# Optimization experiments

Measured on AMD Instinct MI355X. Metric: run time of the kernel, lower is better.

## Reference

```python
import jax, jax.numpy as jnp
import numpy as np

K = 1023   # kernel_size == embedding_dim
H = 16     # out_channels (filters per sample)
E = 256    # num_embeddings
T = 8      # num_tokens
CC = 0.25  # commitment cost
EPS = np.float32(np.finfo(np.float32).eps)
DN = ('NCH', 'OIH', 'NCH')


def setup_inputs() -> dict:
    key = jax.random.key(0)
    ks = jax.random.split(key, 10)
    B, C, L = 8, 1, 8184
    D_ff = 2 * E
    X = jax.random.normal(ks[0], (B, C, L), jnp.float32)
    embedding = jax.random.uniform(ks[1], (E, K), jnp.float32, -1.0 / E, 1.0 / E)
    ffn_w1 = jax.random.normal(ks[2], (E, D_ff), jnp.float32) * 0.02
    ffn_b1 = jnp.zeros((D_ff,), jnp.float32)
    ffn_w2 = jax.random.normal(ks[3], (D_ff, E), jnp.float32) * 0.02
    ffn_b2 = jnp.zeros((E,), jnp.float32)
    ln_g = jnp.ones((E,), jnp.float32)
    ln_b = jnp.zeros((E,), jnp.float32)
    cls_w = jax.random.normal(ks[4], (E, 10), jnp.float32) * 0.02
    cls_b = jnp.zeros((10,), jnp.float32)
    return dict(X=X, embedding=embedding, ffn_w1=ffn_w1, ffn_b1=ffn_b1,
                ffn_w2=ffn_w2, ffn_b2=ffn_b2, ln_g=ln_g, ln_b=ln_b,
                cls_w=cls_w, cls_b=cls_b)


def _autocov(f):
    # f: [..., K]. FFT-based autocovariance of hann-windowed, max-normalized frame.
    n = f.shape[-1]
    fmax = jnp.max(jnp.abs(f), axis=-1, keepdims=True)
    fmax = jnp.where(fmax == 0, EPS, fmax)
    win = 0.5 * (1.0 - jnp.cos(2.0 * jnp.pi * jnp.arange(n, dtype=jnp.float32) / n))
    xw = f * win / fmax
    spec = jnp.abs(jnp.fft.rfft(xw, n=n) ** 2)   # |rfft(x)^2| == |rfft(x)|^2
    return jnp.fft.ifftshift(jnp.fft.irfft(spec, n=n), axes=-1)


def reference(X, embedding, ffn_w1, ffn_b1, ffn_w2, ffn_b2, ln_g, ln_b, cls_w, cls_b):
    B, C, L = X.shape
    # ---- encoder: extract frames at fixed linspace positions, autocovariance ----
    Lp = ((L + K - 1) // K) * K          # PadForConv(zero) length (no-op here)
    end = Lp - K - 1 - K
    positions = jnp.linspace(0.0, float(end), H).astype(jnp.int32)
    idx = positions[:, None] + jnp.arange(K)          # (H, K)
    frames = X[:, :, idx]                             # (B, C, H, K) gather
    Z = _autocov(jnp.transpose(frames, (0, 2, 1, 3)))  # (B, H, C, K)
    # ---- VQ: pairwise distances + argmin + codebook lookup ----
    flat = Z.reshape(-1, K)                           # (B*H*C, K)
    d = (jnp.sum(flat ** 2, axis=1, keepdims=True)
         + jnp.sum(embedding ** 2, axis=1)
         - 2.0 * flat @ embedding.T)                  # (B*H*C, E)
    codes = jnp.argmin(d, axis=1)
    enc = jax.nn.one_hot(codes, E, dtype=flat.dtype)
    quant = (enc @ embedding).reshape(Z.shape)
    sg = jax.lax.stop_gradient
    e_loss = jnp.mean((sg(quant) - Z) ** 2)
    q_loss = jnp.mean((quant - sg(Z)) ** 2)
    vq_loss = q_loss + CC * e_loss
    quant_st = Z + sg(quant - Z)                      # straight-through
    avg = jnp.mean(enc, axis=0)
    perplexity = jnp.exp(-jnp.sum(avg * jnp.log(avg + EPS)))
    # ---- decoder: every sample's filter bank convolved with the whole batch ----
    fmerged = quant_st.reshape(B * H, C, K)           # merge per-sample banks
    out = jax.lax.conv_general_dilated(X, fmerged, (1,), 'SAME',
                                       dimension_numbers=DN)  # (B, B*H, L)
    out = out.reshape(B, B, H, L)                     # (batch b, filter-sample i, k, L)
    sq = (out - X[:, None, :, :]) ** 2                # C==1 broadcast
    # sum_i mean_k mse_{b,l} == mean over (b,k,l) then sum over i
    recon_loss = jnp.sum(jnp.mean(sq, axis=(0, 2, 3)))
    # ---- project: conv with codebook as filters ----
    pfilt = jnp.broadcast_to(embedding[:, None, :], (E, C, K))
    proj = jax.lax.conv_general_dilated(X, pfilt, (1,), 'VALID',
                                        dimension_numbers=DN)  # (B, E, Lo)
    Lo = proj.shape[-1]
    pad = ((Lo + T - 1) // T) * T - Lo                # PadForConv(mean)
    m = jnp.mean(proj, axis=-1, keepdims=True)
    proj = jnp.concatenate([proj, jnp.broadcast_to(m, (B, E, pad))], axis=-1)
    # ---- classify ----
    x = proj.reshape(B, E, T, -1).transpose(0, 2, 3, 1)  # (B, T, t, E)
    x = jnp.max(x, axis=2)                               # (B, T, E)
    mu = jnp.mean(x, axis=-1, keepdims=True)
    var = jnp.var(x, axis=-1, keepdims=True)
    xn = (x - mu) / jnp.sqrt(var + 1e-5) * ln_g + ln_b
    hdd = jax.nn.relu(xn @ ffn_w1 + ffn_b1) @ ffn_w2 + ffn_b2
    feat = jnp.mean(hdd, axis=1)                         # (B, E)
    logits = feat @ cls_w + cls_b
    return (logits, vq_loss, recon_loss, perplexity)
```

## Files before the change

kernel.cpp:

```cpp
#include <hip/hip_runtime.h>

#define KK 1023
#define LL 8184
#define LO 7162
#define XPS 10240
#define EPSF 1.1920928955078125e-07f
#define NEG_INF (-3.4028234663852886e+38f)

typedef short bf16x8 __attribute__((ext_vector_type(8)));
typedef float f32x4 __attribute__((ext_vector_type(4)));

__device__ __constant__ int c_pos[16] = {0,409,818,1227,1636,2045,2454,2863,
                                         3273,3682,4091,4500,4909,5318,5727,6137};

__device__ __forceinline__ unsigned short f2bf(float f) {
    unsigned u = __float_as_uint(f);
    unsigned r = (u + 0x7FFFu + ((u >> 16) & 1u)) >> 16;
    return (unsigned short)r;
}
__device__ __forceinline__ int fenc(float f) {
    int u = __float_as_int(f);
    return u >= 0 ? u : (~u) ^ 0x80000000;
}
__device__ __forceinline__ float fdec(int k) {
    int u = k >= 0 ? k : ~(k ^ 0x80000000);
    return __int_as_float(u);
}
__device__ __forceinline__ void gl2lds16(const void* g, void* l) {
    __builtin_amdgcn_global_load_lds(
        (const __attribute__((address_space(1))) void*)g,
        (__attribute__((address_space(3))) void*)l, 16, 0, 0);
}

__global__ __launch_bounds__(256) void k_prep(const float* __restrict__ X,
                                              const float* __restrict__ emb,
                                              unsigned short* __restrict__ Xpad,
                                              unsigned short* __restrict__ Xodd,
                                              unsigned short* __restrict__ Ebf,
                                              float* __restrict__ Etf,
                                              float* __restrict__ enorm,
                                              int* __restrict__ hist,
                                              int* __restrict__ cmax) {
    __shared__ float red[256];
    const int q = blockIdx.x;
    const int tid = threadIdx.x;
    if (q < 32) {
        const int b = q >> 2, seg = q & 3;
        for (int i = seg * 2560 + tid; i < (seg + 1) * 2560; i += 256) {
            unsigned short v = 0, vo = 0;
            if (i >= 512 && i < 512 + LL) v = f2bf(X[b * LL + (i - 512)]);
            const int i1 = i + 1;
            if (i1 >= 512 && i1 < 512 + LL) vo = f2bf(X[b * LL + (i1 - 512)]);
            Xpad[b * XPS + i] = v;
            Xodd[b * XPS + i] = vo;
        }
    } else if (q < 288) {
        const int e = q - 32;
        const float* er = emb + e * KK;
        float nrm = 0.f;
        for (int k = tid; k < 1024; k += 256) {
            float v = (k < KK) ? er[k] : 0.f;
            Ebf[e * 1024 + k] = (k < KK) ? f2bf(v) : (unsigned short)0;
            Etf[(k >> 2) * 1024 + e * 4 + (k & 3)] = v;
            nrm = fmaf(v, v, nrm);
        }
        red[tid] = nrm;
        __syncthreads();
        for (int off = 128; off; off >>= 1) {
            if (tid < off) red[tid] += red[tid + off];
            __syncthreads();
        }
        if (tid == 0) enorm[e] = red[0];
    } else {
        const int i = (q - 288) * 256 + tid;
        cmax[i] = INT_MIN;
        if (q == 288) hist[tid] = 0;
    }
}

__global__ __launch_bounds__(256) void k_autocov(const float* __restrict__ X,
                                                 float* __restrict__ Z) {
    __shared__ __align__(16) float xw[2046];
    __shared__ float red[256];
    const int fi = blockIdx.x >> 1, half = blockIdx.x & 1;
    const int b = fi >> 4, h = fi & 15;
    const int tid = threadIdx.x;
    const float* xp = X + b * LL + c_pos[h];

    float lmax = 0.f;
    for (int j = tid; j < KK; j += 256) {
        float v = xp[j];
        xw[j] = v;
        lmax = fmaxf(lmax, fabsf(v));
    }
    red[tid] = lmax;
    __syncthreads();
    for (int off = 128; off; off >>= 1) {
        if (tid < off) red[tid] = fmaxf(red[tid], red[tid + off]);
        __syncthreads();
    }
    float fmx = red[0];
    if (fmx == 0.f) fmx = EPSF;
    __syncthreads();
    for (int j = tid; j < KK; j += 256) {
        float v = xw[j];
        float win = 0.5f * (1.0f - cosf(6.28318530717958647692f * (float)j / 1023.0f));
        float w = v * win / fmx;
        xw[j] = w;
        xw[j + KK] = w;
    }
    __syncthreads();

    const int m2 = half * 512 + 2 * tid;
    const int mh = m2 >> 1;
    const float2* X2 = (const float2*)xw;
    float a0 = 0.f, a1 = 0.f;
    float2 F = X2[mh];
#pragma unroll 4
    for (int jh = 0; jh < 511; ++jh) {
        float2 xj = X2[jh];
        float2 G = X2[mh + jh + 1];
        a0 = fmaf(xj.x, F.x, a0);
        a0 = fmaf(xj.y, F.y, a0);
        a1 = fmaf(xj.x, F.y, a1);
        a1 = fmaf(xj.y, G.x, a1);
        F = G;
    }
    float xt = xw[1022];
    a0 = fmaf(xt, F.x, a0);
    a1 = fmaf(xt, F.y, a1);
    float* zrow = Z + fi * KK;
    int i0 = m2 + 512; if (i0 >= KK) i0 -= KK;
    zrow[i0] = a0;
    if (m2 + 1 < KK) {
        int i1 = m2 + 513; if (i1 >= KK) i1 -= KK;
        zrow[i1] = a1;
    }
}

__global__ __launch_bounds__(256) void k_vq(const float* __restrict__ Z,
                                            const float4* __restrict__ Et4,
                                            const float* __restrict__ enorm,
                                            const float* __restrict__ emb,
                                            int* __restrict__ codes,
                                            int* __restrict__ hist,
                                            float* __restrict__ vq_part) {
    __shared__ float zl[KK];
    __shared__ __align__(16) float zm2[1024];
    __shared__ float rv[256];
    __shared__ int   ri[256];
    const int fi = blockIdx.x, tid = threadIdx.x;
    const float* zrow = Z + fi * KK;
    for (int t = tid; t < 1024; t += 256) {
        float z = (t < KK) ? zrow[t] : 0.f;
        if (t < KK) zl[t] = z;
        zm2[t] = -2.f * z;
    }
    __syncthreads();

    float d = enorm[tid];
    const float4* zp = (const float4*)zm2;
    const float4* ep = Et4 + tid;
#pragma unroll 8
    for (int t4 = 0; t4 < 256; ++t4) {
        float4 ev = ep[t4 * 256];
        float4 zv = zp[t4];
        d = fmaf(zv.x, ev.x, d);
        d = fmaf(zv.y, ev.y, d);
        d = fmaf(zv.z, ev.z, d);
        d = fmaf(zv.w, ev.w, d);
    }
    rv[tid] = d; ri[tid] = tid;
    __syncthreads();
    for (int off = 128; off; off >>= 1) {
        if (tid < off) {
            float v2 = rv[tid + off]; int i2 = ri[tid + off];
            if (v2 < rv[tid] || (v2 == rv[tid] && i2 < ri[tid])) { rv[tid] = v2; ri[tid] = i2; }
        }
        __syncthreads();
    }
    const int code = ri[0];
    if (tid == 0) { codes[fi] = code; atomicAdd(&hist[code], 1); }

    const float* qr = emb + code * KK;
    float s = 0.f;
    for (int t = tid; t < KK; t += 256) { float dd = qr[t] - zl[t]; s += dd * dd; }
    __syncthreads();
    rv[tid] = s;
    __syncthreads();
    for (int off = 128; off; off >>= 1) {
        if (tid < off) rv[tid] += rv[tid + off];
        __syncthreads();
    }
    if (tid == 0) vq_part[fi] = rv[0];
}

__global__ __launch_bounds__(512, 2) void k_gemm(const unsigned short* __restrict__ Xpad,
                                                 const unsigned short* __restrict__ Xodd,
                                                 const unsigned short* __restrict__ Ebf,
                                                 const int* __restrict__ codes,
                                                 const float* __restrict__ X,
                                                 float* __restrict__ psum_part,
                                                 float* __restrict__ recon_part,
                                                 int* __restrict__ cmax) {
    __shared__ __align__(16) unsigned short lds_b[16 * 1536];
    __shared__ __align__(16) unsigned short lds_a[2 * 4096];
    __shared__ float red_s[2][64][4];
    const int tid  = threadIdx.x;
    const int lane = tid & 63;
    const int c = lane & 15, g = lane >> 4;
    const int w = tid >> 6, we = w & 1, wg = w >> 1;

    const int bi = blockIdx.x;
    const bool isproj = bi < 512;
    int b, l0, e0;
    if (isproj) { b = bi >> 6; int r = bi & 63; e0 = (r >> 5) * 128; l0 = (r & 31) * 256; }
    else        { int q = bi - 512; b = q >> 5; e0 = 0; l0 = (q & 31) * 256; }
    const int xw0 = (isproj ? 512 : 0) + l0;

    {
        const unsigned short* base_e = Xpad + b * XPS;
        const unsigned short* base_o = Xodd + b * XPS;
#pragma unroll
        for (int kk = 0; kk < 2; ++kk) {
            const int wdw = 2 * w + kk;
            const unsigned short* src = (wdw & 1) ? (base_o + xw0 + wdw - 1)
                                                  : (base_e + xw0 + wdw);
#pragma unroll
            for (int p = 0; p < 3; ++p)
                gl2lds16(src + p * 512 + lane * 8, lds_b + wdw * 1536 + p * 512 + lane * 8);
        }
    }
    const int r_lds = tid >> 2, q4 = tid & 3;
    const int grow = isproj ? (e0 + r_lds) : codes[r_lds];
    const unsigned short* e_src = Ebf + grow * 1024 + q4 * 8;
    gl2lds16(e_src, lds_a + tid * 8);
    __syncthreads();

    f32x4 acc[4][4];
#pragma unroll
    for (int i = 0; i < 4; ++i)
#pragma unroll
        for (int j = 0; j < 4; ++j) acc[i][j] = (f32x4){0.f, 0.f, 0.f, 0.f};

    const char* lax = (const char*)lds_a;
    const char* lbx = (const char*)lds_b;
    const int boff0 = (wg * 4) * 3072 + 32 * c + 16 * g;
    const int aoff0 = we * 4096 + c * 64 + g * 16;

    for (int s = 0; s < 32; ++s) {
        const int cur = s & 1;
        if (s + 1 < 32)
            gl2lds16(e_src + (s + 1) * 32, lds_a + ((s + 1) & 1) * 4096 + tid * 8);
        const char* ab = lax + cur * 8192 + aoff0;
        bf16x8 af[4];
#pragma unroll
        for (int et = 0; et < 4; ++et) af[et] = *(const bf16x8*)(ab + et * 1024);
#pragma unroll
        for (int ntl = 0; ntl < 4; ++ntl) {
            bf16x8 bfrag = *(const bf16x8*)(lbx + boff0 + ntl * 3072 + 64 * s);
#pragma unroll
            for (int et = 0; et < 4; ++et)
                acc[et][ntl] = __builtin_amdgcn_mfma_f32_16x16x32_bf16(af[et], bfrag, acc[et][ntl], 0, 0, 0);
        }
        __syncthreads();
    }

    const int lseg  = l0 >> 8;
    const int lbase = l0 + wg * 4;
    if (isproj) {
        const int ch0 = lbase / 896;
#pragma unroll
        for (int et = 0; et < 4; ++et) {
#pragma unroll
            for (int r = 0; r < 4; ++r) {
                float ssum = 0.f, m0 = NEG_INF, m1 = NEG_INF;
#pragma unroll
                for (int ntl = 0; ntl < 4; ++ntl) {
                    float v = acc[et][ntl][r];
                    int l = lbase + ntl + 16 * c;
                    bool ok = l < LO;
                    ssum += ok ? v : 0.f;
                    int ch = l / 896;
                    if (ok && ch == ch0) m0 = fmaxf(m0, v);
                    if (ok && ch != ch0) m1 = fmaxf(m1, v);
                }
                ssum += __shfl_xor(ssum, 1); ssum += __shfl_xor(ssum, 2);
                ssum += __shfl_xor(ssum, 4); ssum += __shfl_xor(ssum, 8);
                m0 = fmaxf(m0, __shfl_xor(m0, 1)); m0 = fmaxf(m0, __shfl_xor(m0, 2));
                m0 = fmaxf(m0, __shfl_xor(m0, 4)); m0 = fmaxf(m0, __shfl_xor(m0, 8));
                m1 = fmaxf(m1, __shfl_xor(m1, 1)); m1 = fmaxf(m1, __shfl_xor(m1, 2));
                m1 = fmaxf(m1, __shfl_xor(m1, 4)); m1 = fmaxf(m1, __shfl_xor(m1, 8));
                if (c == 0) {
                    int eidx = et * 16 + g * 4 + r;
                    red_s[we][eidx][wg] = ssum;
                    int e = e0 + we * 64 + eidx;
                    int cb = (b * 256 + e) * 8;
                    if (m0 > NEG_INF && ch0 < 8)     atomicMax(&cmax[cb + ch0], fenc(m0));
                    if (m1 > NEG_INF && ch0 + 1 < 8) atomicMax(&cmax[cb + ch0 + 1], fenc(m1));
                }
            }
        }
    } else {
        float xv[4];
#pragma unroll
        for (int ntl = 0; ntl < 4; ++ntl) {
            int lr = lbase + ntl + 16 * c - 1;
            xv[ntl] = (lr >= 0 && lr < LL) ? X[b * LL + lr] : 0.f;
        }
#pragma unroll
        for (int et = 0; et < 4; ++et) {
#pragma unroll
            for (int r = 0; r < 4; ++r) {
                float ssum = 0.f;
#pragma unroll
                for (int ntl = 0; ntl < 4; ++ntl) {
                    int lr = lbase + ntl + 16 * c - 1;
                    bool ok = (lr >= 0) && (lr < LL);
                    float dd = ok ? (acc[et][ntl][r] - xv[ntl]) : 0.f;
                    ssum += dd * dd;
                }
                ssum += __shfl_xor(ssum, 1); ssum += __shfl_xor(ssum, 2);
                ssum += __shfl_xor(ssum, 4); ssum += __shfl_xor(ssum, 8);
                if (c == 0) red_s[we][et * 16 + g * 4 + r][wg] = ssum;
            }
        }
    }
    __syncthreads();
    if (tid < 128) {
        const int wwe = tid >> 6, eidx = tid & 63;
        float tot = red_s[wwe][eidx][0] + red_s[wwe][eidx][1]
                  + red_s[wwe][eidx][2] + red_s[wwe][eidx][3];
        if (isproj) {
            int e = e0 + wwe * 64 + eidx;
            psum_part[lseg * 2048 + b * 256 + e] = tot;
        } else {
            int f = wwe * 64 + eidx;
            recon_part[(b * 128 + f) * 32 + lseg] = tot;
        }
    }
}

__global__ __launch_bounds__(256) void k_ln(const float* __restrict__ psum_part,
                                            const int* __restrict__ cmax,
                                            const float* __restrict__ ln_g,
                                            const float* __restrict__ ln_b,
                                            float* __restrict__ xn) {
    __shared__ float red[256];
    __shared__ float red2[256];
    const int bt = blockIdx.x;
    const int t = bt & 7;
    const int b = bt >> 3;
    const int e = threadIdx.x;
    const float* ps = psum_part + b * 256 + e;
    float sm = 0.f;
#pragma unroll
    for (int s = 0; s < 32; ++s) sm += ps[s * 2048];
    float m = sm * (1.0f / 7162.0f);
    const int cb = (b * 256 + e) << 3;
    float v = (t < 7) ? fdec(cmax[cb + t]) : fmaxf(fdec(cmax[cb + 7]), m);
    red[e] = v; red2[e] = v * v;
    __syncthreads();
    for (int off = 128; off; off >>= 1) {
        if (e < off) { red[e] += red[e + off]; red2[e] += red2[e + off]; }
        __syncthreads();
    }
    float mu  = red[0] * (1.0f / 256.0f);
    float var = red2[0] * (1.0f / 256.0f) - mu * mu;
    float r = 1.0f / sqrtf(var + 1e-5f);
    xn[bt * 256 + e] = (v - mu) * r * ln_g[e] + ln_b[e];
}

__global__ __launch_bounds__(256) void k_ffn1(const float* __restrict__ xn,
                                              const float* __restrict__ w1,
                                              const float* __restrict__ b1,
                                              float* __restrict__ hbuf) {
    __shared__ float xr[256];
    __shared__ float rv[256];
    const int q = blockIdx.x;
    const int bt = q & 63, jc = q >> 6;
    const int tid = threadIdx.x;
    xr[tid] = xn[bt * 256 + tid];
    __syncthreads();
    const int jj = tid & 63, ks = tid >> 6;
    const int j = jc * 64 + jj;
    const float* wp = w1 + (ks * 64) * 512 + j;
    float a = 0.f;
#pragma unroll
    for (int ee = 0; ee < 64; ++ee) a = fmaf(xr[ks * 64 + ee], wp[ee * 512], a);
    rv[tid] = a;
    __syncthreads();
    if (tid < 64) {
        float s = rv[tid] + rv[tid + 64] + rv[tid + 128] + rv[tid + 192];
        hbuf[bt * 512 + jc * 64 + tid] = fmaxf(s + b1[jc * 64 + tid], 0.f);
    }
}

__global__ __launch_bounds__(256) void k_ffn2(const float* __restrict__ hbuf,
                                              const float* __restrict__ w2,
                                              const float* __restrict__ b2,
                                              float* __restrict__ hdd) {
    __shared__ float hr[512];
    __shared__ float rv[256];
    const int q = blockIdx.x;
    const int bt = q & 63, jc = q >> 6;
    const int tid = threadIdx.x;
    hr[tid] = hbuf[bt * 512 + tid];
    hr[tid + 256] = hbuf[bt * 512 + 256 + tid];
    __syncthreads();
    const int jj = tid & 63, ks = tid >> 6;
    const int e = jc * 64 + jj;
    const float* wp = w2 + (ks * 128) * 256 + e;
    float a = 0.f;
#pragma unroll
    for (int j = 0; j < 128; ++j) a = fmaf(hr[ks * 128 + j], wp[j * 256], a);
    rv[tid] = a;
    __syncthreads();
    if (tid < 64) {
        float s = rv[tid] + rv[tid + 64] + rv[tid + 128] + rv[tid + 192];
        hdd[bt * 256 + jc * 64 + tid] = s + b2[jc * 64 + tid];
    }
}

__global__ __launch_bounds__(256) void k_final(const float* __restrict__ hdd,
                                               const float* __restrict__ cls_w,
                                               const float* __restrict__ cls_b,
                                               const float* __restrict__ recon_part,
                                               const float* __restrict__ vq_part,
                                               const int* __restrict__ hist,
                                               float* __restrict__ out) {
    __shared__ float red[256];
    const int tid = threadIdx.x;
    if (blockIdx.x == 0) {
        __shared__ float feat[8][256];
#pragma unroll
        for (int b2 = 0; b2 < 8; ++b2) {
            float fb = 0.f;
#pragma unroll
            for (int t2 = 0; t2 < 8; ++t2) fb += hdd[(b2 * 8 + t2) * 256 + tid];
            feat[b2][tid] = fb * 0.125f;
        }
        __syncthreads();
        if (tid < 80) {
            const int b = tid / 10, k = tid % 10;
            float a = cls_b[k];
            for (int e = 0; e < 256; ++e) a = fmaf(feat[b][e], cls_w[e * 10 + k], a);
            out[tid] = a;
        }
    } else {
        float s = 0.f;
        for (int i = tid; i < 32768; i += 256) s += recon_part[i];
        red[tid] = s;
        __syncthreads();
        for (int off = 128; off; off >>= 1) { if (tid < off) red[tid] += red[tid + off]; __syncthreads(); }
        if (tid == 0) out[81] = red[0] / 1047552.0f;
        __syncthreads();
        red[tid] = (tid < 128) ? vq_part[tid] : 0.f;
        __syncthreads();
        for (int off = 128; off; off >>= 1) { if (tid < off) red[tid] += red[tid + off]; __syncthreads(); }
        if (tid == 0) out[80] = 1.25f * red[0] / 130944.0f;
        __syncthreads();
        float avg = (float)hist[tid] * (1.0f / 128.0f);
        red[tid] = avg * logf(avg + EPSF);
        __syncthreads();
        for (int off = 128; off; off >>= 1) { if (tid < off) red[tid] += red[tid + off]; __syncthreads(); }
        if (tid == 0) out[82] = expf(-red[0]);
    }
}

extern "C" void kernel_launch(void* const* d_in, const int* in_sizes, int n_in,
                              void* d_out, int out_size, void* d_ws, size_t ws_size,
                              hipStream_t stream) {
    const float* X     = (const float*)d_in[0];
    const float* emb   = (const float*)d_in[1];
    const float* w1    = (const float*)d_in[2];
    const float* b1    = (const float*)d_in[3];
    const float* w2    = (const float*)d_in[4];
    const float* b2    = (const float*)d_in[5];
    const float* ln_g  = (const float*)d_in[6];
    const float* ln_b  = (const float*)d_in[7];
    const float* cls_w = (const float*)d_in[8];
    const float* cls_b = (const float*)d_in[9];
    float* out = (float*)d_out;

    float* Z            = (float*)d_ws;
    float* vq_part      = Z + 130944;
    float* xnbuf        = vq_part + 128;
    float* hdd          = xnbuf + 16384;
    float* psum_part    = hdd + 16384;
    float* recon_part   = psum_part + 65536;
    int*   cmaxb        = (int*)(recon_part + 32768);
    int*   codes        = cmaxb + 16384;
    int*   hist         = codes + 128;
    unsigned short* Xpad = (unsigned short*)(hist + 256);
    unsigned short* Xodd = Xpad + 8 * XPS;
    unsigned short* Ebf  = Xodd + 8 * XPS;
    float* Etf           = (float*)(Ebf + 256 * 1024);
    float* enorm         = Etf + 256 * 1024;
    float* hbuf          = enorm + 256;

    k_prep   <<<dim3(352), dim3(256), 0, stream>>>(X, emb, Xpad, Xodd, Ebf, Etf, enorm, hist, cmaxb);
    k_autocov<<<dim3(256), dim3(256), 0, stream>>>(X, Z);
    k_vq     <<<dim3(128), dim3(256), 0, stream>>>(Z, (const float4*)Etf, enorm, emb, codes, hist, vq_part);
    k_gemm   <<<dim3(768), dim3(512), 0, stream>>>(Xpad, Xodd, Ebf, codes, X, psum_part, recon_part, cmaxb);
    k_ln     <<<dim3(64),  dim3(256), 0, stream>>>(psum_part, cmaxb, ln_g, ln_b, xnbuf);
    k_ffn1   <<<dim3(512), dim3(256), 0, stream>>>(xnbuf, w1, b1, hbuf);
    k_ffn2   <<<dim3(256), dim3(256), 0, stream>>>(hbuf, w2, b2, hdd);
    k_final  <<<dim3(2),   dim3(256), 0, stream>>>(hdd, cls_w, cls_b, recon_part, vq_part, hist, out);
}
```

Baseline: 145.4 us.

## Halve GEMM tile rows to cut LDS and registers and raise occupancy

Shrinks the k_gemm tile from 128 to 64 codebook rows per block and restructures the shifted-X LDS staging into 8 windows of 1280 elements, so each wave holds 2x4 accumulators instead of 4x4. The block count doubles to 1536 and launch bounds request 6 blocks per CU, aiming for more resident waves to hide LDS and global latency. In exchange, each B-fragment is reused across fewer rows, more X data is reloaded per row, and more atomics and partial writes are issued.

```diff
diff --git a/kernel.cpp b/kernel.cpp
--- a/kernel.cpp
+++ b/kernel.cpp
@@ -195,7 +195,7 @@
     if (tid == 0) vq_part[fi] = rv[0];
 }
 
-__global__ __launch_bounds__(512, 2) void k_gemm(const unsigned short* __restrict__ Xpad,
+__global__ __launch_bounds__(512, 6) void k_gemm(const unsigned short* __restrict__ Xpad,
                                                  const unsigned short* __restrict__ Xodd,
                                                  const unsigned short* __restrict__ Ebf,
                                                  const int* __restrict__ codes,
@@ -203,65 +203,64 @@
                                                  float* __restrict__ psum_part,
                                                  float* __restrict__ recon_part,
                                                  int* __restrict__ cmax) {
-    __shared__ __align__(16) unsigned short lds_b[16 * 1536];
-    __shared__ __align__(16) unsigned short lds_a[2 * 4096];
-    __shared__ float red_s[2][64][4];
+    __shared__ __align__(16) unsigned short lds_b[8 * 1280];
+    __shared__ __align__(16) unsigned short lds_a[2 * 2048];
+    __shared__ float red_s[64][4];
     const int tid  = threadIdx.x;
     const int lane = tid & 63;
     const int c = lane & 15, g = lane >> 4;
     const int w = tid >> 6, we = w & 1, wg = w >> 1;
 
     const int bi = blockIdx.x;
-    const bool isproj = bi < 512;
-    int b, l0, e0;
-    if (isproj) { b = bi >> 6; int r = bi & 63; e0 = (r >> 5) * 128; l0 = (r & 31) * 256; }
-    else        { int q = bi - 512; b = q >> 5; e0 = 0; l0 = (q & 31) * 256; }
+    const bool isproj = bi < 1024;
+    int b, l0, row0;
+    if (isproj) { b = bi >> 7; int r = bi & 127; row0 = (r >> 5) * 64; l0 = (r & 31) * 256; }
+    else        { int q = bi - 1024; b = q >> 6; int r = q & 63; row0 = (r >> 5) * 64; l0 = (r & 31) * 256; }
     const int xw0 = (isproj ? 512 : 0) + l0;
 
     {
-        const unsigned short* base_e = Xpad + b * XPS;
-        const unsigned short* base_o = Xodd + b * XPS;
-#pragma unroll
-        for (int kk = 0; kk < 2; ++kk) {
-            const int wdw = 2 * w + kk;
-            const unsigned short* src = (wdw & 1) ? (base_o + xw0 + wdw - 1)
-                                                  : (base_e + xw0 + wdw);
-#pragma unroll
-            for (int p = 0; p < 3; ++p)
-                gl2lds16(src + p * 512 + lane * 8, lds_b + wdw * 1536 + p * 512 + lane * 8);
-        }
-    }
-    const int r_lds = tid >> 2, q4 = tid & 3;
-    const int grow = isproj ? (e0 + r_lds) : codes[r_lds];
-    const unsigned short* e_src = Ebf + grow * 1024 + q4 * 8;
-    gl2lds16(e_src, lds_a + tid * 8);
-    __syncthreads();
-
-    f32x4 acc[4][4];
-#pragma unroll
-    for (int i = 0; i < 4; ++i)
+        const unsigned short* base_e = Xpad + b * XPS + xw0;
+        const unsigned short* base_o = Xodd + b * XPS + xw0;
+        for (int k = tid; k < 1280; k += 512) {
+            const int wdw = k / 160;
+            const int p = k - wdw * 160;
+            const unsigned short* src = (wdw & 1) ? (base_o + wdw - 1 + p * 8)
+                                                  : (base_e + wdw + p * 8);
+            gl2lds16(src, lds_b + k * 8);
+        }
+    }
+    const unsigned short* e_src = nullptr;
+    if (tid < 256) {
+        const int r_lds = tid >> 2, q4 = tid & 3;
+        const int grow = isproj ? (row0 + r_lds) : codes[row0 + r_lds];
+        e_src = Ebf + grow * 1024 + q4 * 8;
+        gl2lds16(e_src, lds_a + tid * 8);
+    }
+    __syncthreads();
+
+    f32x4 acc[2][4];
+#pragma unroll
+    for (int i = 0; i < 2; ++i)
 #pragma unroll
         for (int j = 0; j < 4; ++j) acc[i][j] = (f32x4){0.f, 0.f, 0.f, 0.f};
 
     const char* lax = (const char*)lds_a;
     const char* lbx = (const char*)lds_b;
-    const int boff0 = (wg * 4) * 3072 + 32 * c + 16 * g;
-    const int aoff0 = we * 4096 + c * 64 + g * 16;
+    const int boff0 = (wg & 1) * 10240 + ((wg >> 1) << 4) + 32 * c + 16 * g;
+    const int aoff0 = (we * 32 + c) * 64 + g * 16;
 
     for (int s = 0; s < 32; ++s) {
         const int cur = s & 1;
-        if (s + 1 < 32)
-            gl2lds16(e_src + (s + 1) * 32, lds_a + ((s + 1) & 1) * 4096 + tid * 8);
-        const char* ab = lax + cur * 8192 + aoff0;
-        bf16x8 af[4];
-#pragma unroll
-        for (int et = 0; et < 4; ++et) af[et] = *(const bf16x8*)(ab + et * 1024);
+        if (s + 1 < 32 && tid < 256)
+            gl2lds16(e_src + (s + 1) * 32, lds_a + ((s + 1) & 1) * 2048 + tid * 8);
+        const char* ab = lax + cur * 4096 + aoff0;
+        bf16x8 af0 = *(const bf16x8*)(ab);
+        bf16x8 af1 = *(const bf16x8*)(ab + 1024);
 #pragma unroll
         for (int ntl = 0; ntl < 4; ++ntl) {
-            bf16x8 bfrag = *(const bf16x8*)(lbx + boff0 + ntl * 3072 + 64 * s);
-#pragma unroll
-            for (int et = 0; et < 4; ++et)
-                acc[et][ntl] = __builtin_amdgcn_mfma_f32_16x16x32_bf16(af[et], bfrag, acc[et][ntl], 0, 0, 0);
+            bf16x8 bfrag = *(const bf16x8*)(lbx + boff0 + ntl * 2560 + 64 * s);
+            acc[0][ntl] = __builtin_amdgcn_mfma_f32_16x16x32_bf16(af0, bfrag, acc[0][ntl], 0, 0, 0);
+            acc[1][ntl] = __builtin_amdgcn_mfma_f32_16x16x32_bf16(af1, bfrag, acc[1][ntl], 0, 0, 0);
         }
         __syncthreads();
     }
@@ -271,7 +270,7 @@
     if (isproj) {
         const int ch0 = lbase / 896;
 #pragma unroll
-        for (int et = 0; et < 4; ++et) {
+        for (int et = 0; et < 2; ++et) {
 #pragma unroll
             for (int r = 0; r < 4; ++r) {
                 float ssum = 0.f, m0 = NEG_INF, m1 = NEG_INF;
@@ -292,9 +291,9 @@
                 m1 = fmaxf(m1, __shfl_xor(m1, 1)); m1 = fmaxf(m1, __shfl_xor(m1, 2));
                 m1 = fmaxf(m1, __shfl_xor(m1, 4)); m1 = fmaxf(m1, __shfl_xor(m1, 8));
                 if (c == 0) {
-                    int eidx = et * 16 + g * 4 + r;
-                    red_s[we][eidx][wg] = ssum;
-                    int e = e0 + we * 64 + eidx;
+                    int eidx = we * 32 + et * 16 + g * 4 + r;
+                    red_s[eidx][wg] = ssum;
+                    int e = row0 + eidx;
                     int cb = (b * 256 + e) * 8;
                     if (m0 > NEG_INF && ch0 < 8)     atomicMax(&cmax[cb + ch0], fenc(m0));
                     if (m1 > NEG_INF && ch0 + 1 < 8) atomicMax(&cmax[cb + ch0 + 1], fenc(m1));
@@ -309,7 +308,7 @@
             xv[ntl] = (lr >= 0 && lr < LL) ? X[b * LL + lr] : 0.f;
         }
 #pragma unroll
-        for (int et = 0; et < 4; ++et) {
+        for (int et = 0; et < 2; ++et) {
 #pragma unroll
             for (int r = 0; r < 4; ++r) {
                 float ssum = 0.f;
@@ -322,20 +321,18 @@
                 }
                 ssum += __shfl_xor(ssum, 1); ssum += __shfl_xor(ssum, 2);
                 ssum += __shfl_xor(ssum, 4); ssum += __shfl_xor(ssum, 8);
-                if (c == 0) red_s[we][et * 16 + g * 4 + r][wg] = ssum;
+                if (c == 0) red_s[we * 32 + et * 16 + g * 4 + r][wg] = ssum;
             }
         }
     }
     __syncthreads();
-    if (tid < 128) {
-        const int wwe = tid >> 6, eidx = tid & 63;
-        float tot = red_s[wwe][eidx][0] + red_s[wwe][eidx][1]
-                  + red_s[wwe][eidx][2] + red_s[wwe][eidx][3];
+    if (tid < 64) {
+        float tot = red_s[tid][0] + red_s[tid][1] + red_s[tid][2] + red_s[tid][3];
         if (isproj) {
-            int e = e0 + wwe * 64 + eidx;
+            int e = row0 + tid;
             psum_part[lseg * 2048 + b * 256 + e] = tot;
         } else {
-            int f = wwe * 64 + eidx;
+            int f = row0 + tid;
             recon_part[(b * 128 + f) * 32 + lseg] = tot;
         }
     }
@@ -502,7 +499,7 @@
     k_prep   <<<dim3(352), dim3(256), 0, stream>>>(X, emb, Xpad, Xodd, Ebf, Etf, enorm, hist, cmaxb);
     k_autocov<<<dim3(256), dim3(256), 0, stream>>>(X, Z);
     k_vq     <<<dim3(128), dim3(256), 0, stream>>>(Z, (const float4*)Etf, enorm, emb, codes, hist, vq_part);
-    k_gemm   <<<dim3(768), dim3(512), 0, stream>>>(Xpad, Xodd, Ebf, codes, X, psum_part, recon_part, cmaxb);
+    k_gemm   <<<dim3(1536), dim3(512), 0, stream>>>(Xpad, Xodd, Ebf, codes, X, psum_part, recon_part, cmaxb);
     k_ln     <<<dim3(64),  dim3(256), 0, stream>>>(psum_part, cmaxb, ln_g, ln_b, xnbuf);
     k_ffn1   <<<dim3(512), dim3(256), 0, stream>>>(xnbuf, w1, b1, hbuf);
     k_ffn2   <<<dim3(256), dim3(256), 0, stream>>>(hbuf, w2, b2, hdd);
```

Result: faster. 141.9 us (-2.4%).
